# Performance work log

Hardware: AMD Instinct MI355X
Metric: run time of the kernel (lower is better)

Reference implementation:

```python
import jax, jax.numpy as jnp
import numpy as np

N_NODES = 100000
N_EDGES = 3200000
IN_FEATS = 512
HIDDENS = 256
N_CLASSES = 64
K = 10
ALPHA = 0.1


def setup_inputs() -> dict:
    key = jax.random.key(0)
    k1, k2, k3, k4 = jax.random.split(key, 4)
    features = jax.random.normal(k1, (N_NODES, IN_FEATS), dtype=jnp.float32)
    edge_index = jax.random.randint(k2, (2, N_EDGES), 0, N_NODES, dtype=jnp.int64)
    W1 = jax.random.normal(k3, (IN_FEATS, HIDDENS), dtype=jnp.float32) * (1.0 / np.sqrt(IN_FEATS))
    b1 = jnp.zeros((HIDDENS,), dtype=jnp.float32)
    W2 = jax.random.normal(k4, (HIDDENS, N_CLASSES), dtype=jnp.float32) * (1.0 / np.sqrt(HIDDENS))
    b2 = jnp.zeros((N_CLASSES,), dtype=jnp.float32)
    return {"features": features, "edge_index": edge_index,
            "W1": W1, "b1": b1, "W2": W2, "b2": b2}


def reference(features, edge_index, W1, b1, W2, b2):
    # MLP (dropout=0 -> identity): relu(X W1 + b1) W2 + b2
    h = jax.nn.relu(features @ W1 + b1)      # [N, H]
    h = h @ W2 + b2                          # [N, C]

    src, dst = edge_index[0], edge_index[1]
    ones = jnp.ones((src.shape[0],), dtype=h.dtype)
    out_deg = jax.ops.segment_sum(ones, src, num_segments=N_NODES)
    in_deg = jax.ops.segment_sum(ones, dst, num_segments=N_NODES)
    # symmetric normalization D_out^{-1/2} A D_in^{-1/2}, clamped at 1
    norm_src = jax.lax.rsqrt(jnp.maximum(out_deg, 1.0))
    norm_dst = jax.lax.rsqrt(jnp.maximum(in_deg, 1.0))
    coeff = (norm_src[src] * norm_dst[dst])[:, None]  # [E, 1]

    h0 = h
    for _ in range(K):
        msg = h[src] * coeff                               # gather + scale [E, C]
        agg = jax.ops.segment_sum(msg, dst, num_segments=N_NODES)  # spmm
        h = (1.0 - ALPHA) * agg + ALPHA * h0               # teleport blend
    return h
```

## Files before the change

kernel.cpp:

```cpp
#include <hip/hip_runtime.h>
#include <stdint.h>

#define IN_F 512
#define HID  256
#define CLS  64
#define KPOW 10
#define NPASS 8

typedef unsigned short ushort_t;

typedef __attribute__((ext_vector_type(8))) __bf16    bf16x8;
typedef __attribute__((ext_vector_type(4))) float     f32x4;
typedef __attribute__((ext_vector_type(8))) short     s16x8;
typedef __attribute__((ext_vector_type(8))) _Float16  f16x8;
typedef __attribute__((ext_vector_type(4))) _Float16  f16x4;

__device__ __forceinline__ float b2f(ushort_t u) {
    union { unsigned u; float f; } x; x.u = ((unsigned)u) << 16; return x.f;
}
__device__ __forceinline__ ushort_t f2b(float f) {
    union { float f; unsigned u; } x; x.f = f;
    unsigned u = x.u;
    u += 0x7fffu + ((u >> 16) & 1u);
    return (ushort_t)(u >> 16);
}

__device__ __forceinline__ void gll16(const void* g, void* l) {
    __builtin_amdgcn_global_load_lds(
        (const __attribute__((address_space(1))) unsigned int*)g,
        (__attribute__((address_space(3))) unsigned int*)l, 16, 0, 0);
}

__global__ void k_probe(const ushort_t* __restrict__ feat,
                        const int* __restrict__ eidx,
                        int* __restrict__ flags) {
    if (threadIdx.x == 0 && blockIdx.x == 0) {
        int sane = 0;
        for (int i = 0; i < 128; ++i) {
            unsigned u = (unsigned)feat[2 * i] & 0x7fffu;
            unsigned e = u >> 7;
            if (u == 0u || (e >= 100u && e <= 140u)) sane++;
        }
        flags[0] = (sane == 128) ? 0 : 1;
        int nz = 0;
        for (int i = 0; i < 128; ++i) nz |= eidx[2 * i + 1];
        flags[1] = (nz == 0) ? 1 : 0;
    }
}

__device__ __forceinline__ int edge_at(const int* __restrict__ e, long long i, int wide) {
    return wide ? (int)(((const long long*)e)[i]) : e[i];
}

__global__ void k_pack(const int* __restrict__ eidx, int E,
                       int* __restrict__ es32, int* __restrict__ ed32,
                       unsigned* __restrict__ oc, unsigned* __restrict__ ic,
                       const int* __restrict__ flags) {
    const int wide = flags[1];
    int e = blockIdx.x * blockDim.x + threadIdx.x;
    if (e < E) {
        const int s = edge_at(eidx, e, wide);
        const int d = edge_at(eidx, (long long)E + e, wide);
        es32[e] = s;
        ed32[e] = d;
        atomicAdd(&oc[s], 1u);
        atomicAdd(&ic[d], 1u);
    }
}

__global__ void k_norm(const unsigned* __restrict__ oc, const unsigned* __restrict__ ic,
                       float* __restrict__ ns, float* __restrict__ nd9, int N) {
    int i = blockIdx.x * blockDim.x + threadIdx.x;
    if (i < N) {
        ns[i]  = rsqrtf(fmaxf((float)oc[i], 1.0f));
        nd9[i] = 0.9f * rsqrtf(fmaxf((float)ic[i], 1.0f));
    }
}

__global__ void k_scan(const unsigned* __restrict__ cnt, int n,
                       int* __restrict__ offs, int* __restrict__ cursor) {
    __shared__ unsigned ws[16];
    __shared__ unsigned tot;
    const int t    = threadIdx.x;
    const int lane = t & 63;
    const int wid  = t >> 6;
    unsigned carry = 0;
    for (int base = 0; base < n; base += 1024) {
        const int i = base + t;
        const unsigned v = (i < n) ? cnt[i] : 0u;
        unsigned x = v;
        #pragma unroll
        for (int d = 1; d < 64; d <<= 1) {
            unsigned y = __shfl_up(x, d);
            if (lane >= d) x += y;
        }
        if (lane == 63) ws[wid] = x;
        __syncthreads();
        if (wid == 0) {
            const unsigned wv = (lane < 16) ? ws[lane] : 0u;
            unsigned wx = wv;
            #pragma unroll
            for (int d = 1; d < 16; d <<= 1) {
                unsigned y = __shfl_up(wx, d);
                if (lane >= d) wx += y;
            }
            if (lane < 16) ws[lane] = wx - wv;
            if (lane == 15) tot = wx;
        }
        __syncthreads();
        if (i < n) {
            const int o = (int)(carry + ws[wid] + (x - v));
            offs[i]   = o;
            cursor[i] = o;
        }
        carry += tot;
        __syncthreads();
    }
    if (t == 0) offs[n] = (int)carry;
}

__global__ __launch_bounds__(256) void k_scatter_mp(const int* __restrict__ es32,
                                                    const int* __restrict__ ed32,
                                                    int E, int* __restrict__ cursor,
                                                    int* __restrict__ esrc,
                                                    int range, int bpp) {
    const int pass = blockIdx.x / bpp;
    const int b    = blockIdx.x % bpp;
    const int lo   = pass * range;
    const int hi   = lo + range;

    const int stride = bpp * 256 * 4;
    for (int e = (b * 256 + threadIdx.x) * 4; e + 3 < E; e += stride) {
        const int4 d = *(const int4*)&ed32[e];
        const int4 s = *(const int4*)&es32[e];
        if (d.x >= lo && d.x < hi) esrc[atomicAdd(&cursor[d.x], 1)] = s.x;
        if (d.y >= lo && d.y < hi) esrc[atomicAdd(&cursor[d.y], 1)] = s.y;
        if (d.z >= lo && d.z < hi) esrc[atomicAdd(&cursor[d.z], 1)] = s.z;
        if (d.w >= lo && d.w < hi) esrc[atomicAdd(&cursor[d.w], 1)] = s.w;
    }
    if (blockIdx.x == gridDim.x - 1 && threadIdx.x < (E & 3)) {
        const int e = (E & ~3) + threadIdx.x;
        const int d = ed32[e];
        esrc[atomicAdd(&cursor[d], 1)] = es32[e];
    }
}

__global__ void k_prepw(const void* __restrict__ W1, const void* __restrict__ W2,
                        const void* __restrict__ b1, const void* __restrict__ b2,
                        ushort_t* __restrict__ W1t, ushort_t* __restrict__ W2t,
                        float* __restrict__ bias1, float* __restrict__ bias2,
                        const int* __restrict__ flags) {
    const int f32 = flags[0];
    const int stride = gridDim.x * blockDim.x;
    int t = blockIdx.x * blockDim.x + threadIdx.x;
    for (int i = t; i < IN_F * HID; i += stride) {
        int k = i / HID, n = i % HID;
        float v = f32 ? ((const float*)W1)[i] : b2f(((const ushort_t*)W1)[i]);
        W1t[(size_t)n * IN_F + k] = f2b(v);
    }
    for (int i = t; i < HID * CLS; i += stride) {
        int k = i / CLS, n = i % CLS;
        float v = f32 ? ((const float*)W2)[i] : b2f(((const ushort_t*)W2)[i]);
        W2t[(size_t)n * HID + k] = f2b(v);
    }
    if (t < HID) bias1[t] = f32 ? ((const float*)b1)[t] : b2f(((const ushort_t*)b1)[t]);
    if (t < CLS) bias2[t] = f32 ? ((const float*)b2)[t] : b2f(((const ushort_t*)b2)[t]);
}

template<int BM, int BN, int WM, int WN, int MF, int NF, bool RELU, bool OUT_BF16, bool A_DYN>
__global__ __launch_bounds__(256) void k_gemm_mfma(const void* __restrict__ Xv,
                                                   const ushort_t* __restrict__ Wt,
                                                   const float* __restrict__ biasf,
                                                   void* __restrict__ Cv,
                                                   int M, int K,
                                                   const int* __restrict__ flags) {
    __shared__ ushort_t Ws[BN * 64];
    __shared__ ushort_t Xs[BM * 64];

    const bool xF32 = A_DYN ? (flags[0] != 0) : false;
    const int tid  = threadIdx.x;
    const int lane = tid & 63;
    const int wid  = tid >> 6;
    const int wr   = wid / WN;
    const int wc   = wid % WN;
    const int l15  = lane & 15;
    const int lhi  = lane >> 4;
    const int mbase = blockIdx.x * BM;

    f32x4 acc[MF][NF];
    #pragma unroll
    for (int mf = 0; mf < MF; ++mf)
        #pragma unroll
        for (int nf = 0; nf < NF; ++nf)
            acc[mf][nf] = (f32x4){0.f, 0.f, 0.f, 0.f};

    for (int kt = 0; kt < K; kt += 64) {
        constexpr int CW = (BN * 8) / 256;
        #pragma unroll
        for (int i = 0; i < CW; ++i) {
            const int cid = i * 256 + tid;
            const int n   = cid >> 3;
            const int c   = (cid & 7) ^ (n & 7);
            const ushort_t* src = Wt + (size_t)n * K + kt + c * 8;
            void* dst = (void*)((char*)Ws + (size_t)(i * 256 + wid * 64) * 16);
            gll16((const void*)src, dst);
        }
        constexpr int CX = (BM * 8) / 256;
        #pragma unroll
        for (int i = 0; i < CX; ++i) {
            const int cid = i * 256 + tid;
            const int m   = cid >> 3;
            const int c0  = cid & 7;
            int gr = mbase + m; if (gr >= M) gr = M - 1;
            s16x8 val;
            if (xF32) {
                const float* xp = (const float*)Xv + (size_t)gr * K + kt + c0 * 8;
                const float4 f0 = *(const float4*)(xp);
                const float4 f1 = *(const float4*)(xp + 4);
                val[0] = (short)f2b(f0.x); val[1] = (short)f2b(f0.y);
                val[2] = (short)f2b(f0.z); val[3] = (short)f2b(f0.w);
                val[4] = (short)f2b(f1.x); val[5] = (short)f2b(f1.y);
                val[6] = (short)f2b(f1.z); val[7] = (short)f2b(f1.w);
            } else {
                val = *(const s16x8*)((const ushort_t*)Xv + (size_t)gr * K + kt + c0 * 8);
            }
            *(s16x8*)&Xs[(size_t)(m * 8 + (c0 ^ (m & 7))) * 8] = val;
        }
        __syncthreads();

        #pragma unroll
        for (int ks = 0; ks < 2; ++ks) {
            const int k4 = ks * 4 + lhi;
            bf16x8 wf[NF];
            bf16x8 xf[MF];
            #pragma unroll
            for (int nf = 0; nf < NF; ++nf) {
                const int n = wc * (NF * 16) + nf * 16 + l15;
                wf[nf] = *(const bf16x8*)&Ws[(size_t)(n * 8 + (k4 ^ (n & 7))) * 8];
            }
            #pragma unroll
            for (int mf = 0; mf < MF; ++mf) {
                const int m = wr * (MF * 16) + mf * 16 + l15;
                xf[mf] = *(const bf16x8*)&Xs[(size_t)(m * 8 + (k4 ^ (m & 7))) * 8];
            }
            #pragma unroll
            for (int mf = 0; mf < MF; ++mf)
                #pragma unroll
                for (int nf = 0; nf < NF; ++nf)
                    acc[mf][nf] = __builtin_amdgcn_mfma_f32_16x16x32_bf16(
                        wf[nf], xf[mf], acc[mf][nf], 0, 0, 0);
        }
        __syncthreads();
    }

    #pragma unroll
    for (int nf = 0; nf < NF; ++nf) {
        const int nb = wc * (NF * 16) + nf * 16 + lhi * 4;
        const float4 bb = *(const float4*)&biasf[nb];
        #pragma unroll
        for (int mf = 0; mf < MF; ++mf) {
            const int row = mbase + wr * (MF * 16) + mf * 16 + l15;
            if (row < M) {
                float v0 = acc[mf][nf][0] + bb.x;
                float v1 = acc[mf][nf][1] + bb.y;
                float v2 = acc[mf][nf][2] + bb.z;
                float v3 = acc[mf][nf][3] + bb.w;
                if (RELU) {
                    v0 = fmaxf(v0, 0.f); v1 = fmaxf(v1, 0.f);
                    v2 = fmaxf(v2, 0.f); v3 = fmaxf(v3, 0.f);
                }
                if (OUT_BF16) {
                    ushort4 o;
                    o.x = f2b(v0); o.y = f2b(v1); o.z = f2b(v2); o.w = f2b(v3);
                    *(ushort4*)((ushort_t*)Cv + (size_t)row * BN + nb) = o;
                } else {
                    *(float4*)((float*)Cv + (size_t)row * BN + nb) = make_float4(v0, v1, v2, v3);
                }
            }
        }
    }
}

__global__ void k_init(float* __restrict__ h0a0, _Float16* __restrict__ g0,
                       const float* __restrict__ ns, int total4) {
    int i = blockIdx.x * blockDim.x + threadIdx.x;
    if (i < total4) {
        const int base = i * 4;
        float4 v = *(const float4*)&h0a0[base];
        const float s = ns[base >> 6];
        f16x4 o;
        o[0] = (_Float16)(s * v.x); o[1] = (_Float16)(s * v.y);
        o[2] = (_Float16)(s * v.z); o[3] = (_Float16)(s * v.w);
        *(f16x4*)&g0[base] = o;
        *(float4*)&h0a0[base] = make_float4(0.1f * v.x, 0.1f * v.y, 0.1f * v.z, 0.1f * v.w);
    }
}

template<bool LAST>
__global__ __launch_bounds__(256) void k_prop(const _Float16* __restrict__ g,
                                              const float* __restrict__ a0,
                                              const int* __restrict__ esrc,
                                              const int* __restrict__ offs,
                                              const float* __restrict__ nd9,
                                              const float* __restrict__ ns,
                                              void* __restrict__ out, int N) {
    const int lane = threadIdx.x & 63;
    const int wid  = threadIdx.x >> 6;
    const int v    = blockIdx.x * 4 + wid;
    if (v >= N) return;

    const int sub = lane >> 3;
    const int q8  = (lane & 7) << 3;
    const int start = offs[v];
    const int end   = offs[v + 1];

    float aA[8] = {0.f,0.f,0.f,0.f,0.f,0.f,0.f,0.f};
    float aB[8] = {0.f,0.f,0.f,0.f,0.f,0.f,0.f,0.f};
    float aC[8] = {0.f,0.f,0.f,0.f,0.f,0.f,0.f,0.f};
    float aD[8] = {0.f,0.f,0.f,0.f,0.f,0.f,0.f,0.f};

    int i = start;
    for (; i + 32 <= end; i += 32) {
        const int s0 = esrc[i + sub];
        const int s1 = esrc[i + 8  + sub];
        const int s2 = esrc[i + 16 + sub];
        const int s3 = esrc[i + 24 + sub];
        const f16x8 r0 = *(const f16x8*)&g[(size_t)s0 * CLS + q8];
        const f16x8 r1 = *(const f16x8*)&g[(size_t)s1 * CLS + q8];
        const f16x8 r2 = *(const f16x8*)&g[(size_t)s2 * CLS + q8];
        const f16x8 r3 = *(const f16x8*)&g[(size_t)s3 * CLS + q8];
        #pragma unroll
        for (int j = 0; j < 8; ++j) {
            aA[j] += (float)r0[j]; aB[j] += (float)r1[j];
            aC[j] += (float)r2[j]; aD[j] += (float)r3[j];
        }
    }
    if (i + 16 <= end) {
        const int s0 = esrc[i + sub];
        const int s1 = esrc[i + 8 + sub];
        const f16x8 r0 = *(const f16x8*)&g[(size_t)s0 * CLS + q8];
        const f16x8 r1 = *(const f16x8*)&g[(size_t)s1 * CLS + q8];
        #pragma unroll
        for (int j = 0; j < 8; ++j) { aA[j] += (float)r0[j]; aB[j] += (float)r1[j]; }
        i += 16;
    }
    if (i + 8 <= end) {
        const int s0 = esrc[i + sub];
        const f16x8 r0 = *(const f16x8*)&g[(size_t)s0 * CLS + q8];
        #pragma unroll
        for (int j = 0; j < 8; ++j) aC[j] += (float)r0[j];
        i += 8;
    }
    if (i < end && sub < end - i) {
        const int s0 = esrc[i + sub];
        const f16x8 r0 = *(const f16x8*)&g[(size_t)s0 * CLS + q8];
        #pragma unroll
        for (int j = 0; j < 8; ++j) aD[j] += (float)r0[j];
    }

    float r[8];
    #pragma unroll
    for (int j = 0; j < 8; ++j) {
        float x = (aA[j] + aB[j]) + (aC[j] + aD[j]);
        x += __shfl_xor(x, 8);
        x += __shfl_xor(x, 16);
        x += __shfl_xor(x, 32);
        r[j] = x;
    }

    if (sub == 0) {
        const size_t idx = (size_t)v * CLS + q8;
        const float c = nd9[v];
        const float4 t0 = *(const float4*)&a0[idx];
        const float4 t1 = *(const float4*)&a0[idx + 4];
        float h0 = fmaf(c, r[0], t0.x);
        float h1 = fmaf(c, r[1], t0.y);
        float h2 = fmaf(c, r[2], t0.z);
        float h3 = fmaf(c, r[3], t0.w);
        float h4 = fmaf(c, r[4], t1.x);
        float h5 = fmaf(c, r[5], t1.y);
        float h6 = fmaf(c, r[6], t1.z);
        float h7 = fmaf(c, r[7], t1.w);
        if (LAST) {
            float* po = (float*)out + idx;
            *(float4*)(po)     = make_float4(h0, h1, h2, h3);
            *(float4*)(po + 4) = make_float4(h4, h5, h6, h7);
        } else {
            const float s = ns[v];
            f16x8 o;
            o[0] = (_Float16)(s * h0); o[1] = (_Float16)(s * h1);
            o[2] = (_Float16)(s * h2); o[3] = (_Float16)(s * h3);
            o[4] = (_Float16)(s * h4); o[5] = (_Float16)(s * h5);
            o[6] = (_Float16)(s * h6); o[7] = (_Float16)(s * h7);
            *(f16x8*)((_Float16*)out + idx) = o;
        }
    }
}

extern "C" void kernel_launch(void* const* d_in, const int* in_sizes, int n_in,
                              void* d_out, int out_size, void* d_ws, size_t ws_size,
                              hipStream_t stream) {
    const ushort_t* feat = (const ushort_t*)d_in[0];
    const int*      eidx = (const int*)d_in[1];
    const void*     W1   = d_in[2];
    const void*     b1   = d_in[3];
    const void*     W2   = d_in[4];
    const void*     b2   = d_in[5];

    const int N = in_sizes[0] / IN_F;
    const int E = in_sizes[1] / 2;

    char* w = (char*)d_ws;
    auto take = [&](size_t bytes) -> char* {
        char* p = w; w += (bytes + 255) & ~(size_t)255; return p;
    };
    int*      flags = (int*)take(256);
    unsigned* oc    = (unsigned*)take((size_t)N * 4);
    unsigned* ic    = (unsigned*)take((size_t)N * 4);
    float*    ns    = (float*)take((size_t)N * 4);
    float*    nd9   = (float*)take((size_t)N * 4);
    int*      offs  = (int*)take((size_t)(N + 1) * 4);
    int*      curs  = (int*)take((size_t)N * 4);
    int*      esrc  = (int*)take((size_t)E * 4);
    ushort_t* W1t   = (ushort_t*)take((size_t)HID * IN_F * 2);
    ushort_t* W2t   = (ushort_t*)take((size_t)CLS * HID * 2);
    float*    bias1 = (float*)take((size_t)HID * 4);
    float*    bias2 = (float*)take((size_t)CLS * 4);
    float*    h0a0  = (float*)take((size_t)N * CLS * 4);
    char*     regG  = take((size_t)N * HID * 2);
    ushort_t* H1 = (ushort_t*)regG;
    _Float16* gA = (_Float16*)regG;
    _Float16* gB = (_Float16*)(regG + (size_t)N * CLS * 2);

    int* es32;
    if ((size_t)E * 8 <= (size_t)N * CLS * 4) es32 = (int*)h0a0;
    else                                      es32 = (int*)take((size_t)E * 8);
    int* ed32 = es32 + E;

    hipMemsetAsync(oc, 0, (size_t)N * 4, stream);
    hipMemsetAsync(ic, 0, (size_t)N * 4, stream);

    k_probe<<<1, 64, 0, stream>>>(feat, eidx, flags);
    k_prepw<<<256, 256, 0, stream>>>(W1, W2, b1, b2, W1t, W2t, bias1, bias2, flags);

    const int gE = (E + 255) / 256;
    k_pack<<<gE, 256, 0, stream>>>(eidx, E, es32, ed32, oc, ic, flags);
    k_norm<<<(N + 255) / 256, 256, 0, stream>>>(oc, ic, ns, nd9, N);
    k_scan<<<1, 1024, 0, stream>>>(ic, N, offs, curs);

    const int range = (N + NPASS - 1) / NPASS;
    const int bpp   = 800;
    k_scatter_mp<<<NPASS * bpp, 256, 0, stream>>>(es32, ed32, E, curs, esrc, range, bpp);

    k_gemm_mfma<64, 256, 1, 4, 4, 4, true, true, true>
        <<<(N + 63) / 64, 256, 0, stream>>>(feat, W1t, bias1, (void*)H1, N, IN_F, flags);
    k_gemm_mfma<128, 64, 2, 2, 4, 2, false, false, false>
        <<<(N + 127) / 128, 256, 0, stream>>>(H1, W2t, bias2, (void*)h0a0, N, HID, flags);

    const int total4 = (N * CLS) / 4;
    k_init<<<(total4 + 255) / 256, 256, 0, stream>>>(h0a0, gA, ns, total4);

    const int gp = (N + 3) / 4;
    for (int it = 0; it < KPOW; ++it) {
        const _Float16* gin = (it & 1) ? gB : gA;
        if (it == KPOW - 1) {
            k_prop<true ><<<gp, 256, 0, stream>>>(gin, h0a0, esrc, offs, nd9, ns, d_out, N);
        } else {
            _Float16* gout = (it & 1) ? gA : gB;
            k_prop<false><<<gp, 256, 0, stream>>>(gin, h0a0, esrc, offs, nd9, ns, (void*)gout, N);
        }
    }
}
```

Measured before the change: 1.529 ms.

## Fuse MLP GEMMs with edge packing, merge scatter with init, sort adjacency lists

Merges the two MLP GEMMs into one kernel that keeps the hidden activations in shared memory. Extra blocks in the same launch do the edge packing and degree counting. The CSR scatter and the h0 scaling/init run as one launch, and h0*alpha is stored in fp16 instead of fp32 to cut propagation traffic. A new pass sorts each node's neighbour list (up to 64 entries) to improve gather locality, at the cost of an extra kernel and somewhat lower precision on the teleport term.

```diff
diff --git a/kernel.cpp b/kernel.cpp
--- a/kernel.cpp
+++ b/kernel.cpp
@@ -6,6 +6,8 @@
 #define CLS  64
 #define KPOW 10
 #define NPASS 8
+#define BPP   800
+#define PBLK  2048
 
 typedef unsigned short ushort_t;
 
@@ -52,20 +54,26 @@
     return wide ? (int)(((const long long*)e)[i]) : e[i];
 }
 
-__global__ void k_pack(const int* __restrict__ eidx, int E,
-                       int* __restrict__ es32, int* __restrict__ ed32,
-                       unsigned* __restrict__ oc, unsigned* __restrict__ ic,
-                       const int* __restrict__ flags) {
-    const int wide = flags[1];
-    int e = blockIdx.x * blockDim.x + threadIdx.x;
-    if (e < E) {
-        const int s = edge_at(eidx, e, wide);
-        const int d = edge_at(eidx, (long long)E + e, wide);
-        es32[e] = s;
-        ed32[e] = d;
-        atomicAdd(&oc[s], 1u);
-        atomicAdd(&ic[d], 1u);
-    }
+__global__ void k_prepw(const void* __restrict__ W1, const void* __restrict__ W2,
+                        const void* __restrict__ b1, const void* __restrict__ b2,
+                        ushort_t* __restrict__ W1t, ushort_t* __restrict__ W2t,
+                        float* __restrict__ bias1, float* __restrict__ bias2,
+                        const int* __restrict__ flags) {
+    const int f32 = flags[0];
+    const int stride = gridDim.x * blockDim.x;
+    int t = blockIdx.x * blockDim.x + threadIdx.x;
+    for (int i = t; i < IN_F * HID; i += stride) {
+        int k = i / HID, n = i % HID;
+        float v = f32 ? ((const float*)W1)[i] : b2f(((const ushort_t*)W1)[i]);
+        W1t[(size_t)n * IN_F + k] = f2b(v);
+    }
+    for (int i = t; i < HID * CLS; i += stride) {
+        int k = i / CLS, n = i % CLS;
+        float v = f32 ? ((const float*)W2)[i] : b2f(((const ushort_t*)W2)[i]);
+        W2t[(size_t)n * HID + k] = f2b(v);
+    }
+    if (t < HID) bias1[t] = f32 ? ((const float*)b1)[t] : b2f(((const ushort_t*)b1)[t]);
+    if (t < CLS) bias2[t] = f32 ? ((const float*)b2)[t] : b2f(((const ushort_t*)b2)[t]);
 }
 
 __global__ void k_norm(const unsigned* __restrict__ oc, const unsigned* __restrict__ ic,
@@ -119,102 +127,76 @@
     if (t == 0) offs[n] = (int)carry;
 }
 
-__global__ __launch_bounds__(256) void k_scatter_mp(const int* __restrict__ es32,
-                                                    const int* __restrict__ ed32,
-                                                    int E, int* __restrict__ cursor,
-                                                    int* __restrict__ esrc,
-                                                    int range, int bpp) {
-    const int pass = blockIdx.x / bpp;
-    const int b    = blockIdx.x % bpp;
-    const int lo   = pass * range;
-    const int hi   = lo + range;
-
-    const int stride = bpp * 256 * 4;
-    for (int e = (b * 256 + threadIdx.x) * 4; e + 3 < E; e += stride) {
-        const int4 d = *(const int4*)&ed32[e];
-        const int4 s = *(const int4*)&es32[e];
-        if (d.x >= lo && d.x < hi) esrc[atomicAdd(&cursor[d.x], 1)] = s.x;
-        if (d.y >= lo && d.y < hi) esrc[atomicAdd(&cursor[d.y], 1)] = s.y;
-        if (d.z >= lo && d.z < hi) esrc[atomicAdd(&cursor[d.z], 1)] = s.z;
-        if (d.w >= lo && d.w < hi) esrc[atomicAdd(&cursor[d.w], 1)] = s.w;
-    }
-    if (blockIdx.x == gridDim.x - 1 && threadIdx.x < (E & 3)) {
-        const int e = (E & ~3) + threadIdx.x;
-        const int d = ed32[e];
-        esrc[atomicAdd(&cursor[d], 1)] = es32[e];
-    }
-}
-
-__global__ void k_prepw(const void* __restrict__ W1, const void* __restrict__ W2,
-                        const void* __restrict__ b1, const void* __restrict__ b2,
-                        ushort_t* __restrict__ W1t, ushort_t* __restrict__ W2t,
-                        float* __restrict__ bias1, float* __restrict__ bias2,
-                        const int* __restrict__ flags) {
-    const int f32 = flags[0];
-    const int stride = gridDim.x * blockDim.x;
-    int t = blockIdx.x * blockDim.x + threadIdx.x;
-    for (int i = t; i < IN_F * HID; i += stride) {
-        int k = i / HID, n = i % HID;
-        float v = f32 ? ((const float*)W1)[i] : b2f(((const ushort_t*)W1)[i]);
-        W1t[(size_t)n * IN_F + k] = f2b(v);
-    }
-    for (int i = t; i < HID * CLS; i += stride) {
-        int k = i / CLS, n = i % CLS;
-        float v = f32 ? ((const float*)W2)[i] : b2f(((const ushort_t*)W2)[i]);
-        W2t[(size_t)n * HID + k] = f2b(v);
-    }
-    if (t < HID) bias1[t] = f32 ? ((const float*)b1)[t] : b2f(((const ushort_t*)b1)[t]);
-    if (t < CLS) bias2[t] = f32 ? ((const float*)b2)[t] : b2f(((const ushort_t*)b2)[t]);
-}
-
-template<int BM, int BN, int WM, int WN, int MF, int NF, bool RELU, bool OUT_BF16, bool A_DYN>
-__global__ __launch_bounds__(256) void k_gemm_mfma(const void* __restrict__ Xv,
-                                                   const ushort_t* __restrict__ Wt,
-                                                   const float* __restrict__ biasf,
-                                                   void* __restrict__ Cv,
-                                                   int M, int K,
-                                                   const int* __restrict__ flags) {
-    __shared__ ushort_t Ws[BN * 64];
-    __shared__ ushort_t Xs[BM * 64];
-
-    const bool xF32 = A_DYN ? (flags[0] != 0) : false;
-    const int tid  = threadIdx.x;
+__global__ __launch_bounds__(256) void k_fusedA(const void* __restrict__ Xv,
+                                                const ushort_t* __restrict__ W1t,
+                                                const float* __restrict__ bias1,
+                                                const ushort_t* __restrict__ W2t,
+                                                const float* __restrict__ bias2,
+                                                float* __restrict__ h0,
+                                                int M,
+                                                const int* __restrict__ eidx, int E,
+                                                int* __restrict__ es32,
+                                                int* __restrict__ ed32,
+                                                unsigned* __restrict__ oc,
+                                                unsigned* __restrict__ ic,
+                                                const int* __restrict__ flags,
+                                                int nmlp) {
+    __shared__ ushort_t smem[32768];
+    const int bid = blockIdx.x;
+    const int tid = threadIdx.x;
+
+    if (bid >= nmlp) {
+        const int wide = flags[1];
+        const int b = bid - nmlp;
+        for (int e = b * 256 + tid; e < E; e += PBLK * 256) {
+            const int s = edge_at(eidx, e, wide);
+            const int d = edge_at(eidx, (long long)E + e, wide);
+            es32[e] = s;
+            ed32[e] = d;
+            atomicAdd(&oc[s], 1u);
+            atomicAdd(&ic[d], 1u);
+        }
+        return;
+    }
+
+    ushort_t* Ws  = smem;
+    ushort_t* Xs  = smem + 16384;
+    ushort_t* H1s = smem;
+    ushort_t* W2s = smem + 16384;
+
+    const bool xF32 = flags[0] != 0;
     const int lane = tid & 63;
     const int wid  = tid >> 6;
-    const int wr   = wid / WN;
-    const int wc   = wid % WN;
+    const int wc   = wid;
     const int l15  = lane & 15;
     const int lhi  = lane >> 4;
-    const int mbase = blockIdx.x * BM;
-
-    f32x4 acc[MF][NF];
+    const int mbase = bid * 64;
+
+    f32x4 acc1[4][4];
     #pragma unroll
-    for (int mf = 0; mf < MF; ++mf)
-        #pragma unroll
-        for (int nf = 0; nf < NF; ++nf)
-            acc[mf][nf] = (f32x4){0.f, 0.f, 0.f, 0.f};
-
-    for (int kt = 0; kt < K; kt += 64) {
-        constexpr int CW = (BN * 8) / 256;
-        #pragma unroll
-        for (int i = 0; i < CW; ++i) {
+    for (int mf = 0; mf < 4; ++mf)
+        #pragma unroll
+        for (int nf = 0; nf < 4; ++nf)
+            acc1[mf][nf] = (f32x4){0.f, 0.f, 0.f, 0.f};
+
+    for (int kt = 0; kt < IN_F; kt += 64) {
+        #pragma unroll
+        for (int i = 0; i < 8; ++i) {
             const int cid = i * 256 + tid;
             const int n   = cid >> 3;
             const int c   = (cid & 7) ^ (n & 7);
-            const ushort_t* src = Wt + (size_t)n * K + kt + c * 8;
-            void* dst = (void*)((char*)Ws + (size_t)(i * 256 + wid * 64) * 16);
-            gll16((const void*)src, dst);
-        }
-        constexpr int CX = (BM * 8) / 256;
-        #pragma unroll
-        for (int i = 0; i < CX; ++i) {
+            gll16(W1t + (size_t)n * IN_F + kt + c * 8,
+                  (char*)Ws + (size_t)(i * 256 + wid * 64) * 16);
+        }
+        #pragma unroll
+        for (int i = 0; i < 2; ++i) {
             const int cid = i * 256 + tid;
             const int m   = cid >> 3;
             const int c0  = cid & 7;
             int gr = mbase + m; if (gr >= M) gr = M - 1;
             s16x8 val;
             if (xF32) {
-                const float* xp = (const float*)Xv + (size_t)gr * K + kt + c0 * 8;
+                const float* xp = (const float*)Xv + (size_t)gr * IN_F + kt + c0 * 8;
                 const float4 f0 = *(const float4*)(xp);
                 const float4 f1 = *(const float4*)(xp + 4);
                 val[0] = (short)f2b(f0.x); val[1] = (short)f2b(f0.y);
@@ -222,7 +204,7 @@
                 val[4] = (short)f2b(f1.x); val[5] = (short)f2b(f1.y);
                 val[6] = (short)f2b(f1.z); val[7] = (short)f2b(f1.w);
             } else {
-                val = *(const s16x8*)((const ushort_t*)Xv + (size_t)gr * K + kt + c0 * 8);
+                val = *(const s16x8*)((const ushort_t*)Xv + (size_t)gr * IN_F + kt + c0 * 8);
             }
             *(s16x8*)&Xs[(size_t)(m * 8 + (c0 ^ (m & 7))) * 8] = val;
         }
@@ -231,74 +213,153 @@
         #pragma unroll
         for (int ks = 0; ks < 2; ++ks) {
             const int k4 = ks * 4 + lhi;
-            bf16x8 wf[NF];
-            bf16x8 xf[MF];
+            bf16x8 wf[4], xf[4];
             #pragma unroll
-            for (int nf = 0; nf < NF; ++nf) {
-                const int n = wc * (NF * 16) + nf * 16 + l15;
+            for (int nf = 0; nf < 4; ++nf) {
+                const int n = wc * 64 + nf * 16 + l15;
                 wf[nf] = *(const bf16x8*)&Ws[(size_t)(n * 8 + (k4 ^ (n & 7))) * 8];
             }
             #pragma unroll
-            for (int mf = 0; mf < MF; ++mf) {
-                const int m = wr * (MF * 16) + mf * 16 + l15;
+            for (int mf = 0; mf < 4; ++mf) {
+                const int m = mf * 16 + l15;
                 xf[mf] = *(const bf16x8*)&Xs[(size_t)(m * 8 + (k4 ^ (m & 7))) * 8];
             }
             #pragma unroll
-            for (int mf = 0; mf < MF; ++mf)
+            for (int mf = 0; mf < 4; ++mf)
                 #pragma unroll
-                for (int nf = 0; nf < NF; ++nf)
-                    acc[mf][nf] = __builtin_amdgcn_mfma_f32_16x16x32_bf16(
-                        wf[nf], xf[mf], acc[mf][nf], 0, 0, 0);
+                for (int nf = 0; nf < 4; ++nf)
+                    acc1[mf][nf] = __builtin_amdgcn_mfma_f32_16x16x32_bf16(
+                        wf[nf], xf[mf], acc1[mf][nf], 0, 0, 0);
         }
         __syncthreads();
     }
 
     #pragma unroll
-    for (int nf = 0; nf < NF; ++nf) {
-        const int nb = wc * (NF * 16) + nf * 16 + lhi * 4;
-        const float4 bb = *(const float4*)&biasf[nb];
-        #pragma unroll
-        for (int mf = 0; mf < MF; ++mf) {
-            const int row = mbase + wr * (MF * 16) + mf * 16 + l15;
-            if (row < M) {
-                float v0 = acc[mf][nf][0] + bb.x;
-                float v1 = acc[mf][nf][1] + bb.y;
-                float v2 = acc[mf][nf][2] + bb.z;
-                float v3 = acc[mf][nf][3] + bb.w;
-                if (RELU) {
-                    v0 = fmaxf(v0, 0.f); v1 = fmaxf(v1, 0.f);
-                    v2 = fmaxf(v2, 0.f); v3 = fmaxf(v3, 0.f);
-                }
-                if (OUT_BF16) {
-                    ushort4 o;
-                    o.x = f2b(v0); o.y = f2b(v1); o.z = f2b(v2); o.w = f2b(v3);
-                    *(ushort4*)((ushort_t*)Cv + (size_t)row * BN + nb) = o;
-                } else {
-                    *(float4*)((float*)Cv + (size_t)row * BN + nb) = make_float4(v0, v1, v2, v3);
-                }
-            }
-        }
-    }
-}
-
-__global__ void k_init(float* __restrict__ h0a0, _Float16* __restrict__ g0,
-                       const float* __restrict__ ns, int total4) {
-    int i = blockIdx.x * blockDim.x + threadIdx.x;
-    if (i < total4) {
-        const int base = i * 4;
-        float4 v = *(const float4*)&h0a0[base];
-        const float s = ns[base >> 6];
-        f16x4 o;
-        o[0] = (_Float16)(s * v.x); o[1] = (_Float16)(s * v.y);
-        o[2] = (_Float16)(s * v.z); o[3] = (_Float16)(s * v.w);
-        *(f16x4*)&g0[base] = o;
-        *(float4*)&h0a0[base] = make_float4(0.1f * v.x, 0.1f * v.y, 0.1f * v.z, 0.1f * v.w);
-    }
+    for (int nf = 0; nf < 4; ++nf) {
+        const int n0 = wc * 64 + nf * 16 + lhi * 4;
+        const float4 bb = *(const float4*)&bias1[n0];
+        #pragma unroll
+        for (int mf = 0; mf < 4; ++mf) {
+            const int m = mf * 16 + l15;
+            float v0 = fmaxf(acc1[mf][nf][0] + bb.x, 0.f);
+            float v1 = fmaxf(acc1[mf][nf][1] + bb.y, 0.f);
+            float v2 = fmaxf(acc1[mf][nf][2] + bb.z, 0.f);
+            float v3 = fmaxf(acc1[mf][nf][3] + bb.w, 0.f);
+            ushort4 o;
+            o.x = f2b(v0); o.y = f2b(v1); o.z = f2b(v2); o.w = f2b(v3);
+            *(ushort4*)&H1s[(size_t)m * 256 + (size_t)(((n0 >> 3) ^ (m & 7)) * 8) + (n0 & 7)] = o;
+        }
+    }
+    #pragma unroll
+    for (int i = 0; i < 8; ++i) {
+        const int cid = i * 256 + tid;
+        const int n2  = cid >> 5;
+        const int c   = cid & 31;
+        const int csrc = (c & 24) | ((c & 7) ^ (n2 & 7));
+        gll16(W2t + (size_t)n2 * HID + csrc * 8,
+              (char*)W2s + (size_t)(i * 256 + wid * 64) * 16);
+    }
+    __syncthreads();
+
+    f32x4 acc2[4];
+    #pragma unroll
+    for (int nf = 0; nf < 4; ++nf) acc2[nf] = (f32x4){0.f, 0.f, 0.f, 0.f};
+    #pragma unroll
+    for (int ks = 0; ks < 8; ++ks) {
+        const int c = ks * 4 + lhi;
+        const int m = wid * 16 + l15;
+        const bf16x8 xf = *(const bf16x8*)&H1s[(size_t)m * 256 + (size_t)((c ^ (m & 7)) * 8)];
+        #pragma unroll
+        for (int nf = 0; nf < 4; ++nf) {
+            const int n2 = nf * 16 + l15;
+            const bf16x8 wf = *(const bf16x8*)&W2s[(size_t)n2 * 256 + (size_t)((c ^ (n2 & 7)) * 8)];
+            acc2[nf] = __builtin_amdgcn_mfma_f32_16x16x32_bf16(wf, xf, acc2[nf], 0, 0, 0);
+        }
+    }
+    const int row = mbase + wid * 16 + l15;
+    if (row < M) {
+        #pragma unroll
+        for (int nf = 0; nf < 4; ++nf) {
+            const int n2b = nf * 16 + lhi * 4;
+            const float4 bb = *(const float4*)&bias2[n2b];
+            float4 o = make_float4(acc2[nf][0] + bb.x, acc2[nf][1] + bb.y,
+                                   acc2[nf][2] + bb.z, acc2[nf][3] + bb.w);
+            *(float4*)&h0[(size_t)row * CLS + n2b] = o;
+        }
+    }
+}
+
+__global__ __launch_bounds__(256) void k_fusedB(const int* __restrict__ es32,
+                                                const int* __restrict__ ed32,
+                                                int E, int* __restrict__ cursor,
+                                                int* __restrict__ esrc, int range,
+                                                const float* __restrict__ h0,
+                                                _Float16* __restrict__ g0,
+                                                _Float16* __restrict__ a0h,
+                                                const float* __restrict__ ns,
+                                                int total4, int gsc) {
+    const int bid = blockIdx.x;
+    if (bid < gsc) {
+        const int pass = bid / BPP;
+        const int b    = bid % BPP;
+        const int lo   = pass * range;
+        const int hi   = lo + range;
+        const int stride = BPP * 256 * 4;
+        for (int e = (b * 256 + threadIdx.x) * 4; e + 3 < E; e += stride) {
+            const int4 d = *(const int4*)&ed32[e];
+            const int4 s = *(const int4*)&es32[e];
+            if (d.x >= lo && d.x < hi) esrc[atomicAdd(&cursor[d.x], 1)] = s.x;
+            if (d.y >= lo && d.y < hi) esrc[atomicAdd(&cursor[d.y], 1)] = s.y;
+            if (d.z >= lo && d.z < hi) esrc[atomicAdd(&cursor[d.z], 1)] = s.z;
+            if (d.w >= lo && d.w < hi) esrc[atomicAdd(&cursor[d.w], 1)] = s.w;
+        }
+        if (bid == gsc - 1 && threadIdx.x < (E & 3)) {
+            const int e = (E & ~3) + threadIdx.x;
+            const int d = ed32[e];
+            esrc[atomicAdd(&cursor[d], 1)] = es32[e];
+        }
+    } else {
+        const int i = (bid - gsc) * 256 + threadIdx.x;
+        if (i < total4) {
+            const int base = i * 4;
+            const float4 v = *(const float4*)&h0[base];
+            const float s = ns[base >> 6];
+            f16x4 g;
+            g[0] = (_Float16)(s * v.x); g[1] = (_Float16)(s * v.y);
+            g[2] = (_Float16)(s * v.z); g[3] = (_Float16)(s * v.w);
+            *(f16x4*)&g0[base] = g;
+            f16x4 a;
+            a[0] = (_Float16)(0.1f * v.x); a[1] = (_Float16)(0.1f * v.y);
+            a[2] = (_Float16)(0.1f * v.z); a[3] = (_Float16)(0.1f * v.w);
+            *(f16x4*)&a0h[base] = a;
+        }
+    }
+}
+
+__global__ __launch_bounds__(256) void k_sortlist(int* __restrict__ esrc,
+                                                  const int* __restrict__ offs, int N) {
+    const int lane = threadIdx.x & 63;
+    const int wid  = threadIdx.x >> 6;
+    const int v    = blockIdx.x * 4 + wid;
+    if (v >= N) return;
+    const int start = offs[v];
+    const int n     = offs[v + 1] - start;
+    if (n <= 1 || n > 64) return;
+    int x = (lane < n) ? esrc[start + lane] : 0x7fffffff;
+    for (int k = 2; k <= 64; k <<= 1) {
+        for (int j = k >> 1; j >= 1; j >>= 1) {
+            const int y = __shfl_xor(x, j);
+            const bool dir   = (lane & k) == 0;
+            const bool lower = (lane & j) == 0;
+            x = (lower == dir) ? min(x, y) : max(x, y);
+        }
+    }
+    if (lane < n) esrc[start + lane] = x;
 }
 
 template<bool LAST>
 __global__ __launch_bounds__(256) void k_prop(const _Float16* __restrict__ g,
-                                              const float* __restrict__ a0,
+                                              const _Float16* __restrict__ a0h,
                                               const int* __restrict__ esrc,
                                               const int* __restrict__ offs,
                                               const float* __restrict__ nd9,
@@ -371,27 +432,19 @@
     if (sub == 0) {
         const size_t idx = (size_t)v * CLS + q8;
         const float c = nd9[v];
-        const float4 t0 = *(const float4*)&a0[idx];
-        const float4 t1 = *(const float4*)&a0[idx + 4];
-        float h0 = fmaf(c, r[0], t0.x);
-        float h1 = fmaf(c, r[1], t0.y);
-        float h2 = fmaf(c, r[2], t0.z);
-        float h3 = fmaf(c, r[3], t0.w);
-        float h4 = fmaf(c, r[4], t1.x);
-        float h5 = fmaf(c, r[5], t1.y);
-        float h6 = fmaf(c, r[6], t1.z);
-        float h7 = fmaf(c, r[7], t1.w);
+        const f16x8 t = *(const f16x8*)&a0h[idx];
+        float h[8];
+        #pragma unroll
+        for (int j = 0; j < 8; ++j) h[j] = fmaf(c, r[j], (float)t[j]);
         if (LAST) {
             float* po = (float*)out + idx;
-            *(float4*)(po)     = make_float4(h0, h1, h2, h3);
-            *(float4*)(po + 4) = make_float4(h4, h5, h6, h7);
+            *(float4*)(po)     = make_float4(h[0], h[1], h[2], h[3]);
+            *(float4*)(po + 4) = make_float4(h[4], h[5], h[6], h[7]);
         } else {
             const float s = ns[v];
             f16x8 o;
-            o[0] = (_Float16)(s * h0); o[1] = (_Float16)(s * h1);
-            o[2] = (_Float16)(s * h2); o[3] = (_Float16)(s * h3);
-            o[4] = (_Float16)(s * h4); o[5] = (_Float16)(s * h5);
-            o[6] = (_Float16)(s * h6); o[7] = (_Float16)(s * h7);
+            #pragma unroll
+            for (int j = 0; j < 8; ++j) o[j] = (_Float16)(s * h[j]);
             *(f16x8*)((_Float16*)out + idx) = o;
         }
     }
@@ -426,16 +479,13 @@
     ushort_t* W2t   = (ushort_t*)take((size_t)CLS * HID * 2);
     float*    bias1 = (float*)take((size_t)HID * 4);
     float*    bias2 = (float*)take((size_t)CLS * 4);
-    float*    h0a0  = (float*)take((size_t)N * CLS * 4);
-    char*     regG  = take((size_t)N * HID * 2);
-    ushort_t* H1 = (ushort_t*)regG;
-    _Float16* gA = (_Float16*)regG;
-    _Float16* gB = (_Float16*)(regG + (size_t)N * CLS * 2);
-
-    int* es32;
-    if ((size_t)E * 8 <= (size_t)N * CLS * 4) es32 = (int*)h0a0;
-    else                                      es32 = (int*)take((size_t)E * 8);
-    int* ed32 = es32 + E;
+    int*      es32  = (int*)take((size_t)E * 8);
+    int*      ed32  = es32 + E;
+    _Float16* gA    = (_Float16*)take((size_t)N * CLS * 2);
+    _Float16* gB    = (_Float16*)take((size_t)N * CLS * 2);
+    _Float16* a0h   = (_Float16*)take((size_t)N * CLS * 2);
+
+    float* h0 = (float*)d_out;
 
     hipMemsetAsync(oc, 0, (size_t)N * 4, stream);
     hipMemsetAsync(ic, 0, (size_t)N * 4, stream);
@@ -443,31 +493,31 @@
     k_probe<<<1, 64, 0, stream>>>(feat, eidx, flags);
     k_prepw<<<256, 256, 0, stream>>>(W1, W2, b1, b2, W1t, W2t, bias1, bias2, flags);
 
-    const int gE = (E + 255) / 256;
-    k_pack<<<gE, 256, 0, stream>>>(eidx, E, es32, ed32, oc, ic, flags);
+    const int nmlp = (N + 63) / 64;
+    k_fusedA<<<nmlp + PBLK, 256, 0, stream>>>(feat, W1t, bias1, W2t, bias2, h0,
+                                              N, eidx, E, es32, ed32, oc, ic,
+                                              flags, nmlp);
+
     k_norm<<<(N + 255) / 256, 256, 0, stream>>>(oc, ic, ns, nd9, N);
     k_scan<<<1, 1024, 0, stream>>>(ic, N, offs, curs);
 
-    const int range = (N + NPASS - 1) / NPASS;
-    const int bpp   = 800;
-    k_scatter_mp<<<NPASS * bpp, 256, 0, stream>>>(es32, ed32, E, curs, esrc, range, bpp);
-
-    k_gemm_mfma<64, 256, 1, 4, 4, 4, true, true, true>
-        <<<(N + 63) / 64, 256, 0, stream>>>(feat, W1t, bias1, (void*)H1, N, IN_F, flags);
-    k_gemm_mfma<128, 64, 2, 2, 4, 2, false, false, false>
-        <<<(N + 127) / 128, 256, 0, stream>>>(H1, W2t, bias2, (void*)h0a0, N, HID, flags);
-
+    const int range  = (N + NPASS - 1) / NPASS;
+    const int gsc    = NPASS * BPP;
     const int total4 = (N * CLS) / 4;
-    k_init<<<(total4 + 255) / 256, 256, 0, stream>>>(h0a0, gA, ns, total4);
+    const int ginit  = (total4 + 255) / 256;
+    k_fusedB<<<gsc + ginit, 256, 0, stream>>>(es32, ed32, E, curs, esrc, range,
+                                              h0, gA, a0h, ns, total4, gsc);
+
+    k_sortlist<<<(N + 3) / 4, 256, 0, stream>>>(esrc, offs, N);
 
     const int gp = (N + 3) / 4;
     for (int it = 0; it < KPOW; ++it) {
         const _Float16* gin = (it & 1) ? gB : gA;
         if (it == KPOW - 1) {
-            k_prop<true ><<<gp, 256, 0, stream>>>(gin, h0a0, esrc, offs, nd9, ns, d_out, N);
+            k_prop<true ><<<gp, 256, 0, stream>>>(gin, a0h, esrc, offs, nd9, ns, d_out, N);
         } else {
             _Float16* gout = (it & 1) ? gA : gB;
-            k_prop<false><<<gp, 256, 0, stream>>>(gin, h0a0, esrc, offs, nd9, ns, (void*)gout, N);
-        }
-    }
-}
+            k_prop<false><<<gp, 256, 0, stream>>>(gin, a0h, esrc, offs, nd9, ns, (void*)gout, N);
+        }
+    }
+}
```

Result: faster. 1.496 ms (-2.1%).
